# Kernel tuning notes

Measured on AMD Instinct MI355X. Metric: run time of the kernel, lower is better.

## Reference

```python
import jax, jax.numpy as jnp
import numpy as np

N = 50000
E = 800000
D = 64


def setup_inputs() -> dict:
    key = jax.random.key(0)
    ks = jax.random.split(key, 6)
    s = 1.0 / np.sqrt(D)
    return {
        "x": jax.random.normal(ks[0], (N, D), dtype=jnp.float32),
        "edge_index": jax.random.randint(ks[1], (2, E), 0, N, dtype=jnp.int64),
        "W_l1": jax.random.normal(ks[2], (D, D), dtype=jnp.float32) * s,
        "b_l1": jnp.zeros((D,), dtype=jnp.float32),
        "W_r1": jax.random.normal(ks[3], (D, D), dtype=jnp.float32) * s,
        "W_l2": jax.random.normal(ks[4], (D, D), dtype=jnp.float32) * s,
        "b_l2": jnp.zeros((D,), dtype=jnp.float32),
        "W_r2": jax.random.normal(ks[5], (D, D), dtype=jnp.float32) * s,
    }


def _sage_conv(x, src, dst, W_l, b_l, W_r):
    # PyG SAGEConv (aggr='mean'): out = lin_l(mean_{j in N(i)} x_j) + lin_r(x_i)
    msgs = x[src]                                   # [E, D] gather
    agg = jax.ops.segment_sum(msgs, dst, num_segments=N)          # [N, D]
    cnt = jax.ops.segment_sum(jnp.ones((src.shape[0],), x.dtype), dst,
                              num_segments=N)                      # [N]
    agg = agg / jnp.maximum(cnt, 1.0)[:, None]       # mean with deg>=1 guard
    return agg @ W_l.T + b_l + x @ W_r.T


def reference(x, edge_index, W_l1, b_l1, W_r1, W_l2, b_l2, W_r2):
    src, dst = edge_index[0], edge_index[1]
    h = jnp.tanh(_sage_conv(x, src, dst, W_l1, b_l1, W_r1))
    out = _sage_conv(h, src, dst, W_l2, b_l2, W_r2)
    return out
```

## Files before the change

### kernel.cpp

```cpp
#include <hip/hip_runtime.h>
#include <hip/hip_bf16.h>

#define D 64

typedef __attribute__((ext_vector_type(8))) short bf16x8;
typedef __attribute__((ext_vector_type(4))) float f32x4;

__device__ __forceinline__ float bf2f(unsigned short u) {
    return __uint_as_float(((unsigned)u) << 16);
}
__device__ __forceinline__ unsigned short f2bf(float f) {
    __hip_bfloat16 b = __float2bfloat16(f);
    return *(unsigned short*)&b;
}


__global__ void prep_k(const float* __restrict__ x, unsigned short* __restrict__ xbf,
                       const float* __restrict__ Wl1, const float* __restrict__ Wr1,
                       const float* __restrict__ Wl2, const float* __restrict__ Wr2,
                       unsigned short* __restrict__ Wbf,
                       int* __restrict__ cnt, int n4, int ncnt4) {
    int i = blockIdx.x * blockDim.x + threadIdx.x;
    if (i < n4) {
        float4 v = ((const float4*)x)[i];
        ushort4 u;
        u.x = f2bf(v.x); u.y = f2bf(v.y); u.z = f2bf(v.z); u.w = f2bf(v.w);
        ((ushort4*)xbf)[i] = u;
    }
    if (i < ncnt4) ((int4*)cnt)[i] = make_int4(0, 0, 0, 0);
    if (i < 4096) {
        Wbf[i]           = f2bf(Wl1[i]);
        Wbf[4096 + i]    = f2bf(Wr1[i]);
        Wbf[8192 + i]    = f2bf(Wl2[i]);
        Wbf[12288 + i]   = f2bf(Wr2[i]);
    }
}


__global__ void pos_k(const int* __restrict__ dst, int* __restrict__ cnt,
                      int* __restrict__ pos, int E) {
    int e0 = (blockIdx.x * blockDim.x + threadIdx.x) * 4;
    if (e0 + 4 <= E) {
        int4 d = *(const int4*)(dst + e0);
        int4 p;
        p.x = atomicAdd(&cnt[d.x], 1);
        p.y = atomicAdd(&cnt[d.y], 1);
        p.z = atomicAdd(&cnt[d.z], 1);
        p.w = atomicAdd(&cnt[d.w], 1);
        *(int4*)(pos + e0) = p;
    } else {
        for (int e = e0; e < E; ++e) pos[e] = atomicAdd(&cnt[dst[e]], 1);
    }
}

__global__ void scanA_k(const int* __restrict__ cnt, int* __restrict__ rowptr,
                        int* __restrict__ bsum, int N) {
    __shared__ int tmp[256];
    int gid = blockIdx.x * 256 + threadIdx.x;
    int v = (gid < N) ? cnt[gid] : 0;
    tmp[threadIdx.x] = v;
    __syncthreads();
    for (int off = 1; off < 256; off <<= 1) {
        int t = (threadIdx.x >= off) ? tmp[threadIdx.x - off] : 0;
        __syncthreads();
        tmp[threadIdx.x] += t;
        __syncthreads();
    }
    if (gid < N) rowptr[gid] = tmp[threadIdx.x] - v;
    if (threadIdx.x == 255) bsum[blockIdx.x] = tmp[255];
}

__global__ void scanB_k(int* __restrict__ bsum, int nb) {
    __shared__ int tmp[256];
    int v = (threadIdx.x < nb) ? bsum[threadIdx.x] : 0;
    tmp[threadIdx.x] = v;
    __syncthreads();
    for (int off = 1; off < 256; off <<= 1) {
        int t = (threadIdx.x >= off) ? tmp[threadIdx.x - off] : 0;
        __syncthreads();
        tmp[threadIdx.x] += t;
        __syncthreads();
    }
    if (threadIdx.x < nb) bsum[threadIdx.x] = tmp[threadIdx.x] - v;
}

__global__ void scanC_k(int* __restrict__ rowptr, const int* __restrict__ bsum,
                        int N, int E) {
    int gid = blockIdx.x * 256 + threadIdx.x;
    if (gid < N) rowptr[gid] += bsum[blockIdx.x];
    if (blockIdx.x == 0 && threadIdx.x == 0) rowptr[N] = E;
}

__global__ void fill2_k(const int* __restrict__ src, const int* __restrict__ dst,
                        const int* __restrict__ pos, const int* __restrict__ rowptr,
                        unsigned short* __restrict__ col, int E) {
    int e0 = (blockIdx.x * blockDim.x + threadIdx.x) * 4;
    if (e0 + 4 <= E) {
        int4 d = *(const int4*)(dst + e0);
        int4 s = *(const int4*)(src + e0);
        int4 p = *(const int4*)(pos + e0);
        col[rowptr[d.x] + p.x] = (unsigned short)s.x;
        col[rowptr[d.y] + p.y] = (unsigned short)s.y;
        col[rowptr[d.z] + p.z] = (unsigned short)s.z;
        col[rowptr[d.w] + p.w] = (unsigned short)s.w;
    } else {
        for (int e = e0; e < E; ++e)
            col[rowptr[dst[e]] + pos[e]] = (unsigned short)src[e];
    }
}


__device__ __forceinline__ float tanh_fast(float v) {
    float e = __expf(2.f * v);
    return 1.f - 2.f * __builtin_amdgcn_rcpf(e + 1.f);
}

template <int TANH>
__global__ __launch_bounds__(256) void layer_k(
    const unsigned short* __restrict__ xb,
    const int* __restrict__ rowptr, const unsigned short* __restrict__ col,
    const unsigned short* __restrict__ Wlb,
    const unsigned short* __restrict__ Wrb,
    const float* __restrict__ bias,
    float* __restrict__ outf, unsigned short* __restrict__ outb, int N)
{
    __shared__ unsigned short sagg[16][72];
    const int tid = threadIdx.x;
    const int idx = tid & 15;
    const int nl  = tid >> 4;
    const int n0  = blockIdx.x * 16;
    const int n   = n0 + nl;

    if (n < N) {
        const int beg = rowptr[n], end = rowptr[n + 1];
        float ax[8], ay[8], az[8], aw[8];
        #pragma unroll
        for (int s = 0; s < 8; ++s) { ax[s]=0.f; ay[s]=0.f; az[s]=0.f; aw[s]=0.f; }
        int j = beg;
        for (; j + 8 <= end; j += 8) {
            #pragma unroll
            for (int s = 0; s < 8; ++s) {
                int c = col[j + s];
                ushort4 u = *(const ushort4*)(xb + (size_t)c * D + idx * 4);
                ax[s] += bf2f(u.x); ay[s] += bf2f(u.y);
                az[s] += bf2f(u.z); aw[s] += bf2f(u.w);
            }
        }
        for (; j < end; ++j) {
            int c = col[j];
            ushort4 u = *(const ushort4*)(xb + (size_t)c * D + idx * 4);
            ax[0] += bf2f(u.x); ay[0] += bf2f(u.y);
            az[0] += bf2f(u.z); aw[0] += bf2f(u.w);
        }
        float sx = ((ax[0]+ax[1])+(ax[2]+ax[3]))+((ax[4]+ax[5])+(ax[6]+ax[7]));
        float sy = ((ay[0]+ay[1])+(ay[2]+ay[3]))+((ay[4]+ay[5])+(ay[6]+ay[7]));
        float sz = ((az[0]+az[1])+(az[2]+az[3]))+((az[4]+az[5])+(az[6]+az[7]));
        float sw = ((aw[0]+aw[1])+(aw[2]+aw[3]))+((aw[4]+aw[5])+(aw[6]+aw[7]));
        const float inv = 1.0f / fmaxf((float)(end - beg), 1.0f);
        ushort4 o;
        o.x = f2bf(sx*inv); o.y = f2bf(sy*inv); o.z = f2bf(sz*inv); o.w = f2bf(sw*inv);
        *(ushort4*)&sagg[nl][idx * 4] = o;
    } else {
        *(ushort4*)&sagg[nl][idx * 4] = make_ushort4(0, 0, 0, 0);
    }
    __syncthreads();

    const int lane = tid & 63;
    const int wid  = tid >> 6;
    const int fr   = lane & 15;
    const int k0   = (lane >> 4) * 8;
    const int f    = wid * 16 + fr;

    bf16x8 bl[2], br[2];
    {
        const unsigned short* pl = Wlb + f * 64 + k0;
        const unsigned short* pr = Wrb + f * 64 + k0;
        #pragma unroll
        for (int kc = 0; kc < 2; ++kc) {
            bl[kc] = *(const bf16x8*)(pl + kc * 32);
            br[kc] = *(const bf16x8*)(pr + kc * 32);
        }
    }
    float bv = bias[f];
    f32x4 acc = (f32x4){bv, bv, bv, bv};

    bf16x8 aa[2], axf[2];
    #pragma unroll
    for (int kc = 0; kc < 2; ++kc)
        aa[kc] = *(const bf16x8*)&sagg[fr][kc * 32 + k0];
    {
        const unsigned short* px = xb + (size_t)(n0 + fr) * D + k0;
        #pragma unroll
        for (int kc = 0; kc < 2; ++kc)
            axf[kc] = *(const bf16x8*)(px + kc * 32);
    }

    #pragma unroll
    for (int kc = 0; kc < 2; ++kc) {
        acc = __builtin_amdgcn_mfma_f32_16x16x32_bf16(aa[kc],  bl[kc], acc, 0, 0, 0);
        acc = __builtin_amdgcn_mfma_f32_16x16x32_bf16(axf[kc], br[kc], acc, 0, 0, 0);
    }

    const int rbase = n0 + (lane >> 4) * 4;
    #pragma unroll
    for (int r = 0; r < 4; ++r) {
        int node = rbase + r;
        if (node < N) {
            float v = acc[r];
            if (TANH) {
                v = tanh_fast(v);
                outb[(size_t)node * D + f] = f2bf(v);
            } else {
                outf[(size_t)node * D + f] = v;
            }
        }
    }
}


extern "C" void kernel_launch(void* const* d_in, const int* in_sizes, int n_in,
                              void* d_out, int out_size, void* d_ws, size_t ws_size,
                              hipStream_t stream) {
    const float* x   = (const float*)d_in[0];
    const int*   ei  = (const int*)d_in[1];
    const float* Wl1 = (const float*)d_in[2];
    const float* bl1 = (const float*)d_in[3];
    const float* Wr1 = (const float*)d_in[4];
    const float* Wl2 = (const float*)d_in[5];
    const float* bl2 = (const float*)d_in[6];
    const float* Wr2 = (const float*)d_in[7];

    const int N = in_sizes[0] / D;
    const int E = in_sizes[1] / 2;
    const int* srcI = ei;
    const int* dstI = ei + E;

    auto al = [](size_t v) { return (v + 255) & ~(size_t)255; };
    char* w = (char*)d_ws;
    size_t off = 0;
    int*            cnt    = (int*)(w + off);            off += al((size_t)N * 4);
    int*            rowptr = (int*)(w + off);            off += al((size_t)(N + 1) * 4);
    int*            bsum   = (int*)(w + off);            off += al(1024);
    unsigned short* colA   = (unsigned short*)(w + off); off += al((size_t)E * 2);
    unsigned short* xbf    = (unsigned short*)(w + off); off += al((size_t)N * D * 2);
    unsigned short* hbf    = (unsigned short*)(w + off); off += al((size_t)N * D * 2);
    unsigned short* Wbf    = (unsigned short*)(w + off); off += al((size_t)4 * D * D * 2);
    unsigned short* Wb_l1 = Wbf, *Wb_r1 = Wbf + D*D, *Wb_l2 = Wbf + 2*D*D, *Wb_r2 = Wbf + 3*D*D;
    int*            pos    = (int*)(w + off);            off += al((size_t)E * 4);

    float* out = (float*)d_out;

    const int NB  = (N + 255) / 256;
    const int EB4 = (E / 4 + 255) / 256;
    const int PB  = (N * D / 4 + 255) / 256;
    const int LB  = (N + 15) / 16;

    prep_k<<<PB, 256, 0, stream>>>(x, xbf, Wl1, Wr1, Wl2, Wr2, Wbf,
                                   cnt, N * D / 4, (N + 3) / 4);
    pos_k<<<EB4, 256, 0, stream>>>(dstI, cnt, pos, E);
    scanA_k<<<NB, 256, 0, stream>>>(cnt, rowptr, bsum, N);
    scanB_k<<<1, 256, 0, stream>>>(bsum, NB);
    scanC_k<<<NB, 256, 0, stream>>>(rowptr, bsum, N, E);
    fill2_k<<<EB4, 256, 0, stream>>>(srcI, dstI, pos, rowptr, colA, E);

    layer_k<1><<<LB, 256, 0, stream>>>(xbf, rowptr, colA, Wb_l1, Wb_r1, bl1,
                                       nullptr, hbf, N);
    layer_k<0><<<LB, 256, 0, stream>>>(hbf, rowptr, colA, Wb_l2, Wb_r2, bl2,
                                       out, nullptr, N);
}
```

Measured before the change: 130.0 us.

## Drop scanC pass, store positions as u16, mask aggregation tail

Removes the scanC kernel launch. Consumers now add the per-block offset (bsum[n>>8]) to the local row pointer on the fly in fill2_k and layer_k. The pos array shrinks from int32 to uint16, which halves its write and read traffic. The aggregation loop drops its scalar remainder loop and instead runs masked 8-wide iterations with clamped indices, trading some redundant loads for a uniform loop; the u16 positions also assume no node has degree above 65535.

```diff
diff --git a/kernel.cpp b/kernel.cpp
--- a/kernel.cpp
+++ b/kernel.cpp
@@ -38,22 +38,23 @@
 
 
 __global__ void pos_k(const int* __restrict__ dst, int* __restrict__ cnt,
-                      int* __restrict__ pos, int E) {
+                      unsigned short* __restrict__ pos, int E) {
     int e0 = (blockIdx.x * blockDim.x + threadIdx.x) * 4;
     if (e0 + 4 <= E) {
         int4 d = *(const int4*)(dst + e0);
-        int4 p;
-        p.x = atomicAdd(&cnt[d.x], 1);
-        p.y = atomicAdd(&cnt[d.y], 1);
-        p.z = atomicAdd(&cnt[d.z], 1);
-        p.w = atomicAdd(&cnt[d.w], 1);
-        *(int4*)(pos + e0) = p;
+        int px = atomicAdd(&cnt[d.x], 1);
+        int py = atomicAdd(&cnt[d.y], 1);
+        int pz = atomicAdd(&cnt[d.z], 1);
+        int pw = atomicAdd(&cnt[d.w], 1);
+        *(ushort4*)(pos + e0) = make_ushort4((unsigned short)px, (unsigned short)py,
+                                             (unsigned short)pz, (unsigned short)pw);
     } else {
-        for (int e = e0; e < E; ++e) pos[e] = atomicAdd(&cnt[dst[e]], 1);
-    }
-}
-
-__global__ void scanA_k(const int* __restrict__ cnt, int* __restrict__ rowptr,
+        for (int e = e0; e < E; ++e)
+            pos[e] = (unsigned short)atomicAdd(&cnt[dst[e]], 1);
+    }
+}
+
+__global__ void scanA_k(const int* __restrict__ cnt, int* __restrict__ rowptrL,
                         int* __restrict__ bsum, int N) {
     __shared__ int tmp[256];
     int gid = blockIdx.x * 256 + threadIdx.x;
@@ -66,7 +67,7 @@
         tmp[threadIdx.x] += t;
         __syncthreads();
     }
-    if (gid < N) rowptr[gid] = tmp[threadIdx.x] - v;
+    if (gid < N) rowptrL[gid] = tmp[threadIdx.x] - v;
     if (threadIdx.x == 255) bsum[blockIdx.x] = tmp[255];
 }
 
@@ -84,28 +85,22 @@
     if (threadIdx.x < nb) bsum[threadIdx.x] = tmp[threadIdx.x] - v;
 }
 
-__global__ void scanC_k(int* __restrict__ rowptr, const int* __restrict__ bsum,
-                        int N, int E) {
-    int gid = blockIdx.x * 256 + threadIdx.x;
-    if (gid < N) rowptr[gid] += bsum[blockIdx.x];
-    if (blockIdx.x == 0 && threadIdx.x == 0) rowptr[N] = E;
-}
-
 __global__ void fill2_k(const int* __restrict__ src, const int* __restrict__ dst,
-                        const int* __restrict__ pos, const int* __restrict__ rowptr,
+                        const unsigned short* __restrict__ pos,
+                        const int* __restrict__ rowptrL, const int* __restrict__ bsum,
                         unsigned short* __restrict__ col, int E) {
     int e0 = (blockIdx.x * blockDim.x + threadIdx.x) * 4;
     if (e0 + 4 <= E) {
         int4 d = *(const int4*)(dst + e0);
         int4 s = *(const int4*)(src + e0);
-        int4 p = *(const int4*)(pos + e0);
-        col[rowptr[d.x] + p.x] = (unsigned short)s.x;
-        col[rowptr[d.y] + p.y] = (unsigned short)s.y;
-        col[rowptr[d.z] + p.z] = (unsigned short)s.z;
-        col[rowptr[d.w] + p.w] = (unsigned short)s.w;
+        ushort4 p = *(const ushort4*)(pos + e0);
+        col[rowptrL[d.x] + bsum[d.x >> 8] + p.x] = (unsigned short)s.x;
+        col[rowptrL[d.y] + bsum[d.y >> 8] + p.y] = (unsigned short)s.y;
+        col[rowptrL[d.z] + bsum[d.z >> 8] + p.z] = (unsigned short)s.z;
+        col[rowptrL[d.w] + bsum[d.w >> 8] + p.w] = (unsigned short)s.w;
     } else {
         for (int e = e0; e < E; ++e)
-            col[rowptr[dst[e]] + pos[e]] = (unsigned short)src[e];
+            col[rowptrL[dst[e]] + bsum[dst[e] >> 8] + pos[e]] = (unsigned short)src[e];
     }
 }
 
@@ -118,11 +113,12 @@
 template <int TANH>
 __global__ __launch_bounds__(256) void layer_k(
     const unsigned short* __restrict__ xb,
-    const int* __restrict__ rowptr, const unsigned short* __restrict__ col,
+    const int* __restrict__ rowptrL, const int* __restrict__ bsum,
+    const unsigned short* __restrict__ col,
     const unsigned short* __restrict__ Wlb,
     const unsigned short* __restrict__ Wrb,
     const float* __restrict__ bias,
-    float* __restrict__ outf, unsigned short* __restrict__ outb, int N)
+    float* __restrict__ outf, unsigned short* __restrict__ outb, int N, int E)
 {
     __shared__ unsigned short sagg[16][72];
     const int tid = threadIdx.x;
@@ -132,25 +128,24 @@
     const int n   = n0 + nl;
 
     if (n < N) {
-        const int beg = rowptr[n], end = rowptr[n + 1];
+        const int beg = rowptrL[n] + bsum[n >> 8];
+        const int end = (n + 1 < N) ? (rowptrL[n + 1] + bsum[(n + 1) >> 8]) : E;
         float ax[8], ay[8], az[8], aw[8];
         #pragma unroll
         for (int s = 0; s < 8; ++s) { ax[s]=0.f; ay[s]=0.f; az[s]=0.f; aw[s]=0.f; }
-        int j = beg;
-        for (; j + 8 <= end; j += 8) {
+        for (int j = beg; j < end; j += 8) {
             #pragma unroll
             for (int s = 0; s < 8; ++s) {
-                int c = col[j + s];
+                int jj = j + s;
+                float m = (jj < end) ? 1.f : 0.f;
+                jj = (jj < end) ? jj : end - 1;
+                int c = col[jj];
                 ushort4 u = *(const ushort4*)(xb + (size_t)c * D + idx * 4);
-                ax[s] += bf2f(u.x); ay[s] += bf2f(u.y);
-                az[s] += bf2f(u.z); aw[s] += bf2f(u.w);
+                ax[s] = fmaf(m, bf2f(u.x), ax[s]);
+                ay[s] = fmaf(m, bf2f(u.y), ay[s]);
+                az[s] = fmaf(m, bf2f(u.z), az[s]);
+                aw[s] = fmaf(m, bf2f(u.w), aw[s]);
             }
-        }
-        for (; j < end; ++j) {
-            int c = col[j];
-            ushort4 u = *(const ushort4*)(xb + (size_t)c * D + idx * 4);
-            ax[0] += bf2f(u.x); ay[0] += bf2f(u.y);
-            az[0] += bf2f(u.z); aw[0] += bf2f(u.w);
         }
         float sx = ((ax[0]+ax[1])+(ax[2]+ax[3]))+((ax[4]+ax[5])+(ax[6]+ax[7]));
         float sy = ((ay[0]+ay[1])+(ay[2]+ay[3]))+((ay[4]+ay[5])+(ay[6]+ay[7]));
@@ -238,15 +233,15 @@
     auto al = [](size_t v) { return (v + 255) & ~(size_t)255; };
     char* w = (char*)d_ws;
     size_t off = 0;
-    int*            cnt    = (int*)(w + off);            off += al((size_t)N * 4);
-    int*            rowptr = (int*)(w + off);            off += al((size_t)(N + 1) * 4);
-    int*            bsum   = (int*)(w + off);            off += al(1024);
-    unsigned short* colA   = (unsigned short*)(w + off); off += al((size_t)E * 2);
-    unsigned short* xbf    = (unsigned short*)(w + off); off += al((size_t)N * D * 2);
-    unsigned short* hbf    = (unsigned short*)(w + off); off += al((size_t)N * D * 2);
-    unsigned short* Wbf    = (unsigned short*)(w + off); off += al((size_t)4 * D * D * 2);
+    int*            cnt     = (int*)(w + off);            off += al((size_t)N * 4);
+    int*            rowptrL = (int*)(w + off);            off += al((size_t)N * 4);
+    int*            bsum    = (int*)(w + off);            off += al(1024);
+    unsigned short* colA    = (unsigned short*)(w + off); off += al((size_t)E * 2);
+    unsigned short* pos     = (unsigned short*)(w + off); off += al((size_t)E * 2);
+    unsigned short* xbf     = (unsigned short*)(w + off); off += al((size_t)N * D * 2);
+    unsigned short* hbf     = (unsigned short*)(w + off); off += al((size_t)N * D * 2);
+    unsigned short* Wbf     = (unsigned short*)(w + off); off += al((size_t)4 * D * D * 2);
     unsigned short* Wb_l1 = Wbf, *Wb_r1 = Wbf + D*D, *Wb_l2 = Wbf + 2*D*D, *Wb_r2 = Wbf + 3*D*D;
-    int*            pos    = (int*)(w + off);            off += al((size_t)E * 4);
 
     float* out = (float*)d_out;
 
@@ -258,13 +253,12 @@
     prep_k<<<PB, 256, 0, stream>>>(x, xbf, Wl1, Wr1, Wl2, Wr2, Wbf,
                                    cnt, N * D / 4, (N + 3) / 4);
     pos_k<<<EB4, 256, 0, stream>>>(dstI, cnt, pos, E);
-    scanA_k<<<NB, 256, 0, stream>>>(cnt, rowptr, bsum, N);
+    scanA_k<<<NB, 256, 0, stream>>>(cnt, rowptrL, bsum, N);
     scanB_k<<<1, 256, 0, stream>>>(bsum, NB);
-    scanC_k<<<NB, 256, 0, stream>>>(rowptr, bsum, N, E);
-    fill2_k<<<EB4, 256, 0, stream>>>(srcI, dstI, pos, rowptr, colA, E);
-
-    layer_k<1><<<LB, 256, 0, stream>>>(xbf, rowptr, colA, Wb_l1, Wb_r1, bl1,
-                                       nullptr, hbf, N);
-    layer_k<0><<<LB, 256, 0, stream>>>(hbf, rowptr, colA, Wb_l2, Wb_r2, bl2,
-                                       out, nullptr, N);
-}
+    fill2_k<<<EB4, 256, 0, stream>>>(srcI, dstI, pos, rowptrL, bsum, colA, E);
+
+    layer_k<1><<<LB, 256, 0, stream>>>(xbf, rowptrL, bsum, colA, Wb_l1, Wb_r1, bl1,
+                                       nullptr, hbf, N, E);
+    layer_k<0><<<LB, 256, 0, stream>>>(hbf, rowptrL, bsum, colA, Wb_l2, Wb_r2, bl2,
+                                       out, nullptr, N, E);
+}
```

Result: faster. 121.2 us (-6.8%).
